# Kernel tuning notes

Hardware: AMD Instinct MI355X
Metric: run time of the kernel (lower is better)

## Reference

```python
import jax, jax.numpy as jnp
import numpy as np

B, L, H = 4, 256, 768  # batch, seq_len, hidden_size


def setup_inputs() -> dict:
    key = jax.random.key(0)
    k1, k2 = jax.random.split(key, 2)
    seq_hiddens = jax.random.normal(k1, (B, L, H), dtype=jnp.float32)
    # combine_fc: Linear(2*H -> H)
    W = jax.random.normal(k2, (H, 2 * H), dtype=jnp.float32) * 0.02
    b = jnp.zeros((H,), dtype=jnp.float32)
    return {"seq_hiddens": seq_hiddens, "W": W, "b": b}


def reference(seq_hiddens, W, b):
    # Vectorized handshaking ('cat' type): for each pair (i, j) with j >= i,
    # out[p] = tanh(Linear(concat(h_i, h_j))). Pair order matches the torch
    # loop: i ascending, then j ascending (row-major upper triangle).
    L_ = seq_hiddens.shape[1]
    ii, jj = np.triu_indices(L_)          # static index arrays, P = L(L+1)/2
    rep = seq_hiddens[:, ii, :]           # (B, P, H) h_i repeated
    vis = seq_hiddens[:, jj, :]           # (B, P, H) visible suffix hiddens
    x = jnp.concatenate([rep, vis], axis=-1)   # (B, P, 2H)
    out = jnp.tanh(jnp.einsum('bpk,hk->bph', x, W) + b)  # (B, P, H)
    return out
```

## Files before the change

kernel.cpp:

```cpp
#include <hip/hip_runtime.h>
#include <hip/hip_bf16.h>
#include <math.h>

#define B_ 4
#define L_ 256
#define H_ 768
#define P_ 32896
#define N_ 1536
#define K_ 768
#define M_ 1024

typedef __attribute__((ext_vector_type(4))) float f32x4;
typedef __attribute__((ext_vector_type(8))) short s16x8;
typedef const __attribute__((address_space(1))) void* gptr_t;
typedef __attribute__((address_space(3))) void* sptr_t;

__device__ __forceinline__ unsigned pack_bf16(float x, float y) {
    __hip_bfloat16 hx = __float2bfloat16(x);
    __hip_bfloat16 hy = __float2bfloat16(y);
    const unsigned short ux = *(const unsigned short*)&hx;
    const unsigned short uy = *(const unsigned short*)&hy;
    return (unsigned)ux | ((unsigned)uy << 16);
}

__global__ __launch_bounds__(256) void convert_to_bf16(
        const float* __restrict__ A, const float* __restrict__ W,
        unsigned short* __restrict__ Abf, unsigned short* __restrict__ Wbf) {
    const int idx = blockIdx.x * 256 + threadIdx.x;
    const int nA4 = (M_ * K_) / 4;
    const int nW4 = (H_ * N_) / 4;
    if (idx < nA4) {
        const float4 v = ((const float4*)A)[idx];
        ((uint2*)Abf)[idx] = make_uint2(pack_bf16(v.x, v.y), pack_bf16(v.z, v.w));
    } else if (idx < nA4 + nW4) {
        const int wi = idx - nA4;
        const int h  = wi / 384;
        const int c  = (wi % 384) * 4;
        const float4 v = ((const float4*)W)[wi];
        const int n = h + ((c >= 768) ? 768 : 0);
        const int k = (c >= 768) ? (c - 768) : c;
        *(uint2*)(Wbf + (size_t)n * K_ + k) =
            make_uint2(pack_bf16(v.x, v.y), pack_bf16(v.z, v.w));
    }
}

__global__ __launch_bounds__(256) void gemm_uv_bf16(
        const unsigned short* __restrict__ Abf,
        const unsigned short* __restrict__ Wbf,
        const float* __restrict__ bias, float* __restrict__ T) {
    __shared__ __align__(16) char As[64 * 128];
    __shared__ __align__(16) char Bs[64 * 128];

    const int tid  = threadIdx.x;
    const int bm   = blockIdx.x * 64;
    const int bn   = blockIdx.y * 64;
    const int lane = tid & 63;
    const int wave = tid >> 6;

    const int wm  = (wave & 1) * 32;
    const int wn  = (wave >> 1) * 32;
    const int l15 = lane & 15;
    const int l4  = lane >> 4;

    const int rl = lane >> 3;
    const int cc = lane & 7;

    f32x4 acc[2][2] = {};

    for (int kt = 0; kt < K_; kt += 64) {
        __syncthreads();
#pragma unroll
        for (int is = 0; is < 2; ++is) {
            const int r  = wave * 16 + is * 8 + rl;
            const int cp = cc ^ (r & 7);
            __builtin_amdgcn_global_load_lds(
                (gptr_t)(Abf + (size_t)(bm + r) * K_ + kt + cp * 8),
                (sptr_t)(As + (wave * 16 + is * 8) * 128), 16, 0, 0);
            __builtin_amdgcn_global_load_lds(
                (gptr_t)(Wbf + (size_t)(bn + r) * K_ + kt + cp * 8),
                (sptr_t)(Bs + (wave * 16 + is * 8) * 128), 16, 0, 0);
        }
        __syncthreads();
#pragma unroll
        for (int ks = 0; ks < 2; ++ks) {
            s16x8 af[2], bf[2];
#pragma unroll
            for (int mi = 0; mi < 2; ++mi) {
                const int row = wm + mi * 16 + l15;
                const int chunk = (ks * 4 + l4) ^ (row & 7);
                af[mi] = *(const s16x8*)(As + row * 128 + chunk * 16);
            }
#pragma unroll
            for (int ni = 0; ni < 2; ++ni) {
                const int row = wn + ni * 16 + l15;
                const int chunk = (ks * 4 + l4) ^ (row & 7);
                bf[ni] = *(const s16x8*)(Bs + row * 128 + chunk * 16);
            }
#pragma unroll
            for (int mi = 0; mi < 2; ++mi)
#pragma unroll
                for (int ni = 0; ni < 2; ++ni)
                    acc[mi][ni] = __builtin_amdgcn_mfma_f32_16x16x32_bf16(
                        af[mi], bf[ni], acc[mi][ni], 0, 0, 0);
        }
    }

#pragma unroll
    for (int mi = 0; mi < 2; ++mi)
#pragma unroll
        for (int ni = 0; ni < 2; ++ni) {
            const int gm0 = bm + wm + mi * 16 + l4 * 4;
            const int gn  = bn + wn + ni * 16 + l15;
            const float badd = (gn < H_) ? bias[gn] : 0.0f;
#pragma unroll
            for (int r = 0; r < 4; ++r)
                T[(size_t)(gm0 + r) * N_ + gn] = acc[mi][ni][r] + badd;
        }
}

__global__ __launch_bounds__(256) void gemm_uv_mfma(
        const float* __restrict__ A, const float* __restrict__ W,
        const float* __restrict__ bias, float* __restrict__ T) {
    __shared__ __align__(16) char As[64 * 128];
    __shared__ __align__(16) char Bs[64 * 128];

    const int tid = threadIdx.x;
    const int bm = blockIdx.x * 64;
    const int bn = blockIdx.y * 64;
    const int lane = tid & 63;
    const int wave = tid >> 6;

    const int sr = tid >> 4;
    const int sk = (tid & 15) * 4;
    const float* wbase = (bn < H_) ? (W + (size_t)bn * N_)
                                   : (W + (size_t)(bn - H_) * N_ + H_);

    const int wm = (wave & 1) * 32;
    const int wn = (wave >> 1) * 32;
    const int l15 = lane & 15;
    const int l4  = lane >> 4;

    f32x4 acc[2][2] = {};

    for (int kt = 0; kt < K_; kt += 64) {
        __syncthreads();
#pragma unroll
        for (int ph = 0; ph < 4; ++ph) {
            const int row = ph * 16 + sr;
            const float4 av = *(const float4*)(A + (size_t)(bm + row) * K_ + kt + sk);
            const float4 bv = *(const float4*)(wbase + (size_t)row * N_ + kt + sk);
            const int chunk = sk >> 3;
            const int sub   = (sk & 4) ? 8 : 0;
            const int boff  = row * 128 + ((chunk ^ (row & 7)) * 16) + sub;
            *(uint2*)(As + boff) = make_uint2(pack_bf16(av.x, av.y), pack_bf16(av.z, av.w));
            *(uint2*)(Bs + boff) = make_uint2(pack_bf16(bv.x, bv.y), pack_bf16(bv.z, bv.w));
        }
        __syncthreads();
#pragma unroll
        for (int ks = 0; ks < 2; ++ks) {
            s16x8 af[2], bf[2];
#pragma unroll
            for (int mi = 0; mi < 2; ++mi) {
                const int row = wm + mi * 16 + l15;
                const int chunk = (ks * 4 + l4) ^ (row & 7);
                af[mi] = *(const s16x8*)(As + row * 128 + chunk * 16);
            }
#pragma unroll
            for (int ni = 0; ni < 2; ++ni) {
                const int row = wn + ni * 16 + l15;
                const int chunk = (ks * 4 + l4) ^ (row & 7);
                bf[ni] = *(const s16x8*)(Bs + row * 128 + chunk * 16);
            }
#pragma unroll
            for (int mi = 0; mi < 2; ++mi)
#pragma unroll
                for (int ni = 0; ni < 2; ++ni)
                    acc[mi][ni] = __builtin_amdgcn_mfma_f32_16x16x32_bf16(
                        af[mi], bf[ni], acc[mi][ni], 0, 0, 0);
        }
    }

#pragma unroll
    for (int mi = 0; mi < 2; ++mi)
#pragma unroll
        for (int ni = 0; ni < 2; ++ni) {
            const int gm0 = bm + wm + mi * 16 + l4 * 4;
            const int gn  = bn + wn + ni * 16 + l15;
            const float badd = (gn < H_) ? bias[gn] : 0.0f;
#pragma unroll
            for (int r = 0; r < 4; ++r)
                T[(size_t)(gm0 + r) * N_ + gn] = acc[mi][ni][r] + badd;
        }
}

__device__ __forceinline__ float fast_tanh(float x) {
    const float e = __builtin_amdgcn_exp2f(x * 2.885390081777926815f);
    const float r = __builtin_amdgcn_rcpf(e + 1.0f);
    return fmaf(-2.0f, r, 1.0f);
}

__device__ __forceinline__ f32x4 tanh4(f32x4 u, f32x4 v) {
    f32x4 o;
    o.x = fast_tanh(u.x + v.x);
    o.y = fast_tanh(u.y + v.y);
    o.z = fast_tanh(u.z + v.z);
    o.w = fast_tanh(u.w + v.w);
    return o;
}

__global__ __launch_bounds__(192) void handshake_epilogue_seq(
        const float* __restrict__ T,
        float* __restrict__ out) {
    const int bid  = blockIdx.x;
    const int b    = (bid & 7) >> 1;
    const int half = bid & 1;
    const int i1   = bid >> 3;
    const int i2   = 255 - i1;

    const int j_mid = (i1 <= 63) ? (i1 + 128) : 191;
    const int jlo = half ? j_mid : i1;
    const int jhi = half ? 256 : j_mid;

    const int h = threadIdx.x * 4;
    const float* Tb = T + (size_t)b * L_ * N_;
    const float* Vb = Tb + H_ + h;

    const f32x4 u1 = *(const f32x4*)(Tb + (size_t)i1 * N_ + h);
    const f32x4 u2 = *(const f32x4*)(Tb + (size_t)i2 * N_ + h);

    const size_t off1 = (size_t)i1 * (2 * L_ + 1 - i1) / 2;
    const size_t off2 = (size_t)i2 * (2 * L_ + 1 - i2) / 2;
    float* o1 = out + ((size_t)b * P_ + off1 + (size_t)(jlo - i1)) * H_ + h;
    const int j2first = (jlo > i2) ? jlo : i2;
    float* o2 = out + ((size_t)b * P_ + off2 + (size_t)(j2first - i2)) * H_ + h;

    f32x4 v0 = *(const f32x4*)(Vb + (size_t)jlo * N_);
    f32x4 v1 = (jlo + 1 < 256) ? *(const f32x4*)(Vb + (size_t)(jlo + 1) * N_) : v0;

    for (int j = jlo; j < jhi; ++j) {
        const f32x4 vc = v0;
        v0 = v1;
        if (j + 2 < 256)
            v1 = *(const f32x4*)(Vb + (size_t)(j + 2) * N_);

        __builtin_nontemporal_store(tanh4(u1, vc), (f32x4*)o1);
        o1 += H_;
        if (j >= i2) {
            __builtin_nontemporal_store(tanh4(u2, vc), (f32x4*)o2);
            o2 += H_;
        }
    }
}

extern "C" void kernel_launch(void* const* d_in, const int* in_sizes, int n_in,
                              void* d_out, int out_size, void* d_ws, size_t ws_size,
                              hipStream_t stream) {
    const float* seq  = (const float*)d_in[0];
    const float* W    = (const float*)d_in[1];
    const float* bias = (const float*)d_in[2];
    float* out = (float*)d_out;

    char* ws = (char*)d_ws;
    float* T = (float*)ws;
    const size_t T_BYTES = (size_t)M_ * N_ * 4;
    unsigned short* Abf = (unsigned short*)(ws + T_BYTES);
    unsigned short* Wbf = (unsigned short*)(ws + T_BYTES + (size_t)M_ * K_ * 2);
    const size_t NEED = T_BYTES + (size_t)M_ * K_ * 2 + (size_t)K_ * N_ * 2;

    dim3 g1(M_ / 64, N_ / 64);
    if (ws_size >= NEED) {
        convert_to_bf16<<<1920, 256, 0, stream>>>(seq, W, Abf, Wbf);
        gemm_uv_bf16<<<g1, 256, 0, stream>>>(Abf, Wbf, bias, T);
    } else {
        gemm_uv_mfma<<<g1, 256, 0, stream>>>(seq, W, bias, T);
    }

    handshake_epilogue_seq<<<1024, 192, 0, stream>>>(T, out);
}
```

Baseline: 104.7 us.

## Replace per-row-pair epilogue with grid-stride flat output-row epilogue

The epilogue now walks flat output rows (b, p) with a grid-stride loop, recovering (i, j) from p through a sqrt-based triangular inverse with integer correction. Previously each block paired rows i and 255-i and streamed j sequentially, with register prefetch of the V rows. The new mapping keeps adjacent blocks writing contiguous output so stores stay sequential, and it balances work evenly. In exchange it reloads u for every row, adds a sqrt and integer math per row, and gives up the software prefetch of V.

```diff
diff --git a/kernel.cpp b/kernel.cpp
--- a/kernel.cpp
+++ b/kernel.cpp
@@ -208,47 +208,29 @@
     return o;
 }
 
-__global__ __launch_bounds__(192) void handshake_epilogue_seq(
+#define NROWS_ (B_ * P_)
+
+__global__ __launch_bounds__(192) void handshake_epilogue_front(
         const float* __restrict__ T,
         float* __restrict__ out) {
-    const int bid  = blockIdx.x;
-    const int b    = (bid & 7) >> 1;
-    const int half = bid & 1;
-    const int i1   = bid >> 3;
-    const int i2   = 255 - i1;
-
-    const int j_mid = (i1 <= 63) ? (i1 + 128) : 191;
-    const int jlo = half ? j_mid : i1;
-    const int jhi = half ? 256 : j_mid;
-
     const int h = threadIdx.x * 4;
-    const float* Tb = T + (size_t)b * L_ * N_;
-    const float* Vb = Tb + H_ + h;
-
-    const f32x4 u1 = *(const f32x4*)(Tb + (size_t)i1 * N_ + h);
-    const f32x4 u2 = *(const f32x4*)(Tb + (size_t)i2 * N_ + h);
-
-    const size_t off1 = (size_t)i1 * (2 * L_ + 1 - i1) / 2;
-    const size_t off2 = (size_t)i2 * (2 * L_ + 1 - i2) / 2;
-    float* o1 = out + ((size_t)b * P_ + off1 + (size_t)(jlo - i1)) * H_ + h;
-    const int j2first = (jlo > i2) ? jlo : i2;
-    float* o2 = out + ((size_t)b * P_ + off2 + (size_t)(j2first - i2)) * H_ + h;
-
-    f32x4 v0 = *(const f32x4*)(Vb + (size_t)jlo * N_);
-    f32x4 v1 = (jlo + 1 < 256) ? *(const f32x4*)(Vb + (size_t)(jlo + 1) * N_) : v0;
-
-    for (int j = jlo; j < jhi; ++j) {
-        const f32x4 vc = v0;
-        v0 = v1;
-        if (j + 2 < 256)
-            v1 = *(const f32x4*)(Vb + (size_t)(j + 2) * N_);
-
-        __builtin_nontemporal_store(tanh4(u1, vc), (f32x4*)o1);
-        o1 += H_;
-        if (j >= i2) {
-            __builtin_nontemporal_store(tanh4(u2, vc), (f32x4*)o2);
-            o2 += H_;
-        }
+    const int stride = gridDim.x;
+
+    for (int r = blockIdx.x; r < NROWS_; r += stride) {
+        const int b = r / P_;
+        const int p = r - b * P_;
+
+        const float Df = (float)(263169 - 8 * p);
+        int i = (int)((513.0f - __builtin_sqrtf(Df)) * 0.5f);
+        if ((i + 1) * (513 - (i + 1)) / 2 <= p) ++i;
+        if (i * (513 - i) / 2 > p) --i;
+        const int j = p - i * (513 - i) / 2 + i;
+
+        const float* Tb = T + (size_t)b * L_ * N_;
+        const f32x4 u = *(const f32x4*)(Tb + (size_t)i * N_ + h);
+        const f32x4 v = *(const f32x4*)(Tb + (size_t)j * N_ + H_ + h);
+        __builtin_nontemporal_store(tanh4(u, v),
+                                    (f32x4*)(out + (size_t)r * H_ + h));
     }
 }
 
@@ -275,5 +257,5 @@
         gemm_uv_mfma<<<g1, 256, 0, stream>>>(seq, W, bias, T);
     }
 
-    handshake_epilogue_seq<<<1024, 192, 0, stream>>>(T, out);
-}
+    handshake_epilogue_front<<<2048, 192, 0, stream>>>(T, out);
+}
```

Measured after the change: 94.51 us. 9.7% less time.
